# Optimization experiments

Measured on AMD Instinct MI355X. Metric: run time of the kernel, lower is better.

Reference implementation:

```python
import jax, jax.numpy as jnp
import numpy as np

N = 10000
E = 320000
DIM_IN, DIM_H, DIM_OUT, HEADS = 256, 64, 32, 8
NEG_SLOPE = 0.2


def setup_inputs() -> dict:
    key = jax.random.key(0)
    ks = jax.random.split(key, 10)
    x = jax.random.normal(ks[0], (N, DIM_IN), dtype=jnp.float32)
    edge_index = jax.random.randint(ks[1], (2, E), 0, N, dtype=jnp.int64)
    def glorot(k, shape, fan_in):
        return jax.random.normal(k, shape, dtype=jnp.float32) / np.sqrt(fan_in)
    # layer 1: GATv2Conv(256 -> 64, heads=8)
    W1l = glorot(ks[2], (DIM_IN, HEADS * DIM_H), DIM_IN)
    W1r = glorot(ks[3], (DIM_IN, HEADS * DIM_H), DIM_IN)
    att1 = glorot(ks[4], (HEADS, DIM_H), DIM_H)
    b1 = jnp.zeros((HEADS * DIM_H,), dtype=jnp.float32)
    # layer 2: GATv2Conv(512 -> 32, heads=1)
    W2l = glorot(ks[5], (HEADS * DIM_H, DIM_OUT), HEADS * DIM_H)
    W2r = glorot(ks[6], (HEADS * DIM_H, DIM_OUT), HEADS * DIM_H)
    att2 = glorot(ks[7], (1, DIM_OUT), DIM_OUT)
    b2 = jnp.zeros((DIM_OUT,), dtype=jnp.float32)
    return {"x": x, "edge_index": edge_index, "W1l": W1l, "W1r": W1r,
            "att1": att1, "b1": b1, "W2l": W2l, "W2r": W2r, "att2": att2, "b2": b2}


def gatv2_conv(x, src, dst, Wl, Wr, att, bias, heads, out_ch, concat):
    n = x.shape[0]
    xl = (x @ Wl).reshape(n, heads, out_ch)  # source transform
    xr = (x @ Wr).reshape(n, heads, out_ch)  # target transform
    e = jax.nn.leaky_relu(xl[src] + xr[dst], NEG_SLOPE)       # [E,H,C]
    alpha = jnp.einsum('ehc,hc->eh', e, att)                  # [E,H]
    amax = jax.lax.stop_gradient(
        jax.ops.segment_max(alpha, dst, num_segments=n))      # [N,H]
    ex = jnp.exp(alpha - amax[dst])
    denom = jax.ops.segment_sum(ex, dst, num_segments=n)
    alpha = ex / (denom[dst] + 1e-16)
    msg = xl[src] * alpha[..., None]                          # [E,H,C]
    out = jax.ops.segment_sum(msg, dst, num_segments=n)       # [N,H,C]
    out = out.reshape(n, heads * out_ch) if concat else out.mean(axis=1)
    return out + bias


def reference(x, edge_index, W1l, W1r, att1, b1, W2l, W2r, att2, b2):
    n = x.shape[0]
    loops = jnp.arange(n, dtype=edge_index.dtype)
    src = jnp.concatenate([edge_index[0], loops])  # add_self_loops=True (PyG default)
    dst = jnp.concatenate([edge_index[1], loops])
    h = gatv2_conv(x, src, dst, W1l, W1r, att1, b1, HEADS, DIM_H, True)
    h = jax.nn.elu(h)
    h = gatv2_conv(h, src, dst, W2l, W2r, att2, b2, 1, DIM_OUT, True)
    return jax.nn.log_softmax(h, axis=1)
```

## Files before the change

### kernel.cpp

```cpp
#include <hip/hip_runtime.h>
#include <hip/hip_bf16.h>


constexpr int N_NODES = 10000;
constexpr int N_EDGES = 320000;
constexpr int ET      = N_EDGES + N_NODES;
constexpr float NEG_SLOPE = 0.2f;

constexpr int NB_COUNT  = (ET + 255) / 256;
constexpr int NB_CONVX  = (N_NODES * 64) / 256;
constexpr int NB_CONVW  = (1024 * 64) / 256;
constexpr int NB_CONVW2 = (64 * 128) / 256;

typedef __attribute__((ext_vector_type(8))) short short8;
typedef __attribute__((ext_vector_type(8))) unsigned short ushort8_t;
typedef __attribute__((ext_vector_type(4))) float floatx4;

__device__ __forceinline__ float lrelu(float a) {
    return fmaxf(a, NEG_SLOPE * a);
}
__device__ __forceinline__ unsigned short f2bf(float f) {
    unsigned u = __float_as_uint(f);
    unsigned r = u + 0x7FFFu + ((u >> 16) & 1u);
    return (unsigned short)(r >> 16);
}
__device__ __forceinline__ float bf2f(unsigned short h) {
    return __uint_as_float((unsigned)h << 16);
}
__device__ __forceinline__ float red8_dpp(float p) {
    int x;
    x = __builtin_amdgcn_update_dpp(0, __float_as_int(p), 0xB1, 0xF, 0xF, true);
    p += __int_as_float(x);
    x = __builtin_amdgcn_update_dpp(0, __float_as_int(p), 0x4E, 0xF, 0xF, true);
    p += __int_as_float(x);
    x = __builtin_amdgcn_update_dpp(0, __float_as_int(p), 0x141, 0xF, 0xF, true);
    p += __int_as_float(x);
    return p;
}
__device__ __forceinline__ float red8max_dpp(float p) {
    int x;
    x = __builtin_amdgcn_update_dpp(0, __float_as_int(p), 0xB1, 0xF, 0xF, true);
    p = fmaxf(p, __int_as_float(x));
    x = __builtin_amdgcn_update_dpp(0, __float_as_int(p), 0x4E, 0xF, 0xF, true);
    p = fmaxf(p, __int_as_float(x));
    x = __builtin_amdgcn_update_dpp(0, __float_as_int(p), 0x141, 0xF, 0xF, true);
    p = fmaxf(p, __int_as_float(x));
    return p;
}
__device__ __forceinline__ float ror8_add(float p) {
    int x = __builtin_amdgcn_update_dpp(0, __float_as_int(p), 0x128, 0xF, 0xF, true);
    return p + __int_as_float(x);
}


__global__ __launch_bounds__(256) void k_prep(const int* __restrict__ ei,
        int* __restrict__ deg, const float* __restrict__ x,
        unsigned short* __restrict__ A, const float* __restrict__ Wl,
        const float* __restrict__ Wr, unsigned short* __restrict__ Bt,
        const float* __restrict__ W2l, const float* __restrict__ W2r,
        unsigned short* __restrict__ Bt2) {
    int b = blockIdx.x, t = threadIdx.x;
    if (b < NB_COUNT) {
        int e = b * 256 + t;
        if (e >= ET) return;
        int d = (e < N_EDGES) ? ei[N_EDGES + e] : (e - N_EDGES);
        atomicAdd(&deg[d], 1);
    } else if (b < NB_COUNT + NB_CONVX) {
        int idx = (b - NB_COUNT) * 256 + t;
        int m = idx >> 6, kg = (idx & 63) << 2;
        float4 v = *reinterpret_cast<const float4*>(x + (size_t)m * 256 + kg);
        ushort4 hi = make_ushort4(f2bf(v.x), f2bf(v.y), f2bf(v.z), f2bf(v.w));
        ushort4 lo = make_ushort4(f2bf(v.x - bf2f(hi.x)), f2bf(v.y - bf2f(hi.y)),
                                  f2bf(v.z - bf2f(hi.z)), f2bf(v.w - bf2f(hi.w)));
        size_t base = (size_t)m * 512 + kg;
        *reinterpret_cast<ushort4*>(A + base)       = hi;
        *reinterpret_cast<ushort4*>(A + base + 256) = lo;
    } else if (b < NB_COUNT + NB_CONVX + NB_CONVW) {
        int idx = (b - NB_COUNT - NB_CONVX) * 256 + t;
        int n = idx >> 6, kg = (idx & 63) << 2;
        const float* src = (n < 512) ? (Wl + n) : (Wr + (n - 512));
        float v0 = src[(size_t)(kg + 0) * 512];
        float v1 = src[(size_t)(kg + 1) * 512];
        float v2 = src[(size_t)(kg + 2) * 512];
        float v3 = src[(size_t)(kg + 3) * 512];
        ushort4 hi = make_ushort4(f2bf(v0), f2bf(v1), f2bf(v2), f2bf(v3));
        size_t base = (size_t)n * 512 + kg;
        *reinterpret_cast<ushort4*>(Bt + base)       = hi;
        *reinterpret_cast<ushort4*>(Bt + base + 256) = hi;
    } else {
        int idx = (b - NB_COUNT - NB_CONVX - NB_CONVW) * 256 + t;
        int j = idx >> 7, kg = (idx & 127) << 2;
        const float* src = (j < 32) ? (W2l + j) : (W2r + (j - 32));
        float v0 = src[(size_t)(kg + 0) * 32];
        float v1 = src[(size_t)(kg + 1) * 32];
        float v2 = src[(size_t)(kg + 2) * 32];
        float v3 = src[(size_t)(kg + 3) * 32];
        ushort4 hi = make_ushort4(f2bf(v0), f2bf(v1), f2bf(v2), f2bf(v3));
        *reinterpret_cast<ushort4*>(Bt2 + (size_t)j * 512 + kg) = hi;
    }
}


__global__ __launch_bounds__(1024) void k_scan(const int* __restrict__ deg,
                                               int* __restrict__ offs) {
    __shared__ int part[1024];
    const int CH = 10;
    int t = threadIdx.x;
    int base = t * CH;
    int loc[CH];
    int s = 0;
    for (int i = 0; i < CH; ++i) {
        int idx = base + i;
        int v = (idx < N_NODES) ? deg[idx] : 0;
        loc[i] = s; s += v;
    }
    part[t] = s;
    __syncthreads();
    for (int o = 1; o < 1024; o <<= 1) {
        int add = (t >= o) ? part[t - o] : 0;
        __syncthreads();
        part[t] += add;
        __syncthreads();
    }
    int excl = part[t] - s;
    for (int i = 0; i < CH; ++i) {
        int idx = base + i;
        if (idx < N_NODES) offs[idx] = excl + loc[i];
    }
    if (t == 1023) offs[N_NODES] = part[1023];
}

__global__ void k_scatter(const int* __restrict__ ei, const int* __restrict__ offs,
                          int* __restrict__ deg, int* __restrict__ ssrc) {
    int e = blockIdx.x * 256 + threadIdx.x;
    if (e >= ET) return;
    int s, d;
    if (e < N_EDGES) { s = ei[e]; d = ei[N_EDGES + e]; }
    else             { s = d = e - N_EDGES; }
    int pos = offs[d] + atomicAdd(&deg[d], -1) - 1;
    ssrc[pos] = s;
}


__global__ __launch_bounds__(256) void k_mfma1(const unsigned short* __restrict__ A,
        const unsigned short* __restrict__ Bt, unsigned short* __restrict__ xl1b,
        unsigned short* __restrict__ xr1b) {
    __shared__ unsigned short As[128 * 40];
    __shared__ unsigned short Bs[128 * 40];
    int t = threadIdx.x;
    int wave = t >> 6, L = t & 63;
    int wm = wave & 1, wn = wave >> 1;
    int row0 = blockIdx.x * 128, n0 = blockIdx.y * 128;
    int q = L >> 4, rr = L & 15;
    floatx4 acc[4][4];
#pragma unroll
    for (int i = 0; i < 4; ++i)
#pragma unroll
        for (int j = 0; j < 4; ++j) acc[i][j] = (floatx4){0.f, 0.f, 0.f, 0.f};
    int ra = t >> 2,        ka = (t & 3) * 8;
    int rb = (t + 256) >> 2, kb = ((t + 256) & 3) * 8;
    int gma = row0 + ra; gma = (gma < N_NODES) ? gma : (N_NODES - 1);
    int gmb = row0 + rb; gmb = (gmb < N_NODES) ? gmb : (N_NODES - 1);
    for (int kc = 0; kc < 512; kc += 32) {
        __syncthreads();
        *reinterpret_cast<uint4*>(&As[ra * 40 + ka]) =
            *reinterpret_cast<const uint4*>(A + (size_t)gma * 512 + kc + ka);
        *reinterpret_cast<uint4*>(&As[rb * 40 + kb]) =
            *reinterpret_cast<const uint4*>(A + (size_t)gmb * 512 + kc + kb);
        *reinterpret_cast<uint4*>(&Bs[ra * 40 + ka]) =
            *reinterpret_cast<const uint4*>(Bt + (size_t)(n0 + ra) * 512 + kc + ka);
        *reinterpret_cast<uint4*>(&Bs[rb * 40 + kb]) =
            *reinterpret_cast<const uint4*>(Bt + (size_t)(n0 + rb) * 512 + kc + kb);
        __syncthreads();
        short8 af[4], bf[4];
#pragma unroll
        for (int st = 0; st < 4; ++st)
            af[st] = *reinterpret_cast<const short8*>(
                &As[(wm * 64 + st * 16 + rr) * 40 + q * 8]);
#pragma unroll
        for (int st = 0; st < 4; ++st)
            bf[st] = *reinterpret_cast<const short8*>(
                &Bs[(wn * 64 + st * 16 + rr) * 40 + q * 8]);
#pragma unroll
        for (int i = 0; i < 4; ++i)
#pragma unroll
            for (int j = 0; j < 4; ++j)
                acc[i][j] = __builtin_amdgcn_mfma_f32_16x16x32_bf16(
                    af[i], bf[j], acc[i][j], 0, 0, 0);
    }
#pragma unroll
    for (int j = 0; j < 4; ++j) {
        int gc = n0 + wn * 64 + j * 16 + rr;
        unsigned short* dst = (gc < 512) ? xl1b : xr1b;
        int col = (gc < 512) ? gc : (gc - 512);
#pragma unroll
        for (int i = 0; i < 4; ++i)
#pragma unroll
            for (int r = 0; r < 4; ++r) {
                int gr = row0 + wm * 64 + i * 16 + q * 4 + r;
                if (gr < N_NODES)
                    dst[(size_t)gr * 512 + col] = f2bf(acc[i][j][r]);
            }
    }
}

__global__ __launch_bounds__(512) void k_node1f(const int* __restrict__ offs,
        const int* __restrict__ ssrc, const unsigned short* __restrict__ xl1b,
        const unsigned short* __restrict__ xr1b, const float* __restrict__ att1,
        const float* __restrict__ b1, unsigned short* __restrict__ h1b) {
    int n = blockIdx.x;
    int t = threadIdx.x;
    int h = t >> 6, lane = t & 63;
    int beg = offs[n], dcnt = offs[n + 1] - beg;
    int ej = lane >> 3;
    int cg = lane & 7;
    float xrv[8], atv[8];
    {
        ushort8_t xru = *reinterpret_cast<const ushort8_t*>(
            xr1b + (size_t)n * 512 + h * 64 + cg * 8);
        const float* atrow = att1 + h * 64 + cg * 8;
        float4 c0 = *reinterpret_cast<const float4*>(atrow);
        float4 c1 = *reinterpret_cast<const float4*>(atrow + 4);
#pragma unroll
        for (int i = 0; i < 8; ++i) xrv[i] = bf2f(xru[i]);
        atv[0]=c0.x; atv[1]=c0.y; atv[2]=c0.z; atv[3]=c0.w;
        atv[4]=c1.x; atv[5]=c1.y; atv[6]=c1.z; atv[7]=c1.w;
    }
    float l = 0.f;
    float acc8[8];
#pragma unroll
    for (int i = 0; i < 8; ++i) acc8[i] = 0.f;
    const int* sp = ssrc + beg;
    const char* xlbase = reinterpret_cast<const char*>(xl1b) + h * 128 + cg * 16;

    auto ld_off = [&](int i1) -> int {
        int i1c = (i1 < dcnt) ? i1 : (dcnt - 1);
        return sp[i1c] << 10;
    };
    auto ld_row = [&](int off) -> ushort8_t {
        return *reinterpret_cast<const ushort8_t*>(xlbase + off);
    };
    int full = dcnt & ~15;
    ushort8_t uA = ld_row(ld_off(ej));
    ushort8_t uB = ld_row(ld_off(8 + ej));
    int oA1 = ld_off(16 + ej), oB1 = ld_off(24 + ej);
    for (int base = 0; base < full; base += 16) {
        ushort8_t uA1 = ld_row(oA1), uB1 = ld_row(oB1);
        int oA2 = ld_off(base + 32 + ej);
        int oB2 = ld_off(base + 40 + ej);
        float xsA[8], xsB[8];
#pragma unroll
        for (int i = 0; i < 8; ++i) { xsA[i] = bf2f(uA[i]); xsB[i] = bf2f(uB[i]); }
        float pA0 = 0.f, pA1 = 0.f, pB0 = 0.f, pB1 = 0.f;
#pragma unroll
        for (int i = 0; i < 4; ++i) {
            pA0 += lrelu(xsA[i] + xrv[i]) * atv[i];
            pA1 += lrelu(xsA[i + 4] + xrv[i + 4]) * atv[i + 4];
            pB0 += lrelu(xsB[i] + xrv[i]) * atv[i];
            pB1 += lrelu(xsB[i + 4] + xrv[i + 4]) * atv[i + 4];
        }
        float wA = __expf(fminf(red8_dpp(pA0 + pA1), 60.f));
        float wB = __expf(fminf(red8_dpp(pB0 + pB1), 60.f));
        l += wA + wB;
#pragma unroll
        for (int i = 0; i < 8; ++i) acc8[i] += wA * xsA[i] + wB * xsB[i];
        uA = uA1; uB = uB1; oA1 = oA2; oB1 = oB2;
    }
    if (full < dcnt) {
        float xsA[8], xsB[8];
#pragma unroll
        for (int i = 0; i < 8; ++i) { xsA[i] = bf2f(uA[i]); xsB[i] = bf2f(uB[i]); }
        float pA0 = 0.f, pA1 = 0.f, pB0 = 0.f, pB1 = 0.f;
#pragma unroll
        for (int i = 0; i < 4; ++i) {
            pA0 += lrelu(xsA[i] + xrv[i]) * atv[i];
            pA1 += lrelu(xsA[i + 4] + xrv[i + 4]) * atv[i + 4];
            pB0 += lrelu(xsB[i] + xrv[i]) * atv[i];
            pB1 += lrelu(xsB[i + 4] + xrv[i + 4]) * atv[i + 4];
        }
        float pA = red8_dpp(pA0 + pA1);
        float pB = red8_dpp(pB0 + pB1);
        if (full + ej >= dcnt)     pA = -1e30f;
        if (full + 8 + ej >= dcnt) pB = -1e30f;
        float wA = __expf(fminf(pA, 60.f));
        float wB = __expf(fminf(pB, 60.f));
        l += wA + wB;
#pragma unroll
        for (int i = 0; i < 8; ++i) acc8[i] += wA * xsA[i] + wB * xsB[i];
    }
    l = ror8_add(l); l += __shfl_xor(l, 16); l += __shfl_xor(l, 32);
#pragma unroll
    for (int i = 0; i < 8; ++i) {
        acc8[i] = ror8_add(acc8[i]);
        acc8[i] += __shfl_xor(acc8[i], 16);
        acc8[i] += __shfl_xor(acc8[i], 32);
    }
    float inv = 1.f / (l + 1e-16f);
    if (ej == 0) {
        const float* brow = b1 + h * 64 + cg * 8;
        ushort8_t vout;
#pragma unroll
        for (int i = 0; i < 8; ++i) {
            float v = acc8[i] * inv + brow[i];
            v = (v > 0.f) ? v : (__expf(v) - 1.f);
            vout[i] = f2bf(v);
        }
        *reinterpret_cast<ushort8_t*>(
            h1b + (size_t)n * 512 + h * 64 + cg * 8) = vout;
    }
}


__global__ __launch_bounds__(256) void k_mfma2(const unsigned short* __restrict__ h1b,
        const unsigned short* __restrict__ Bt2, float* __restrict__ xw2) {
    __shared__ unsigned short Hs[128 * 40];
    __shared__ unsigned short Ws[64 * 40];
    int t = threadIdx.x;
    int wave = t >> 6, L = t & 63;
    int row0 = blockIdx.x * 128;
    int q = L >> 4, rr = L & 15;
    floatx4 acc[2][4];
#pragma unroll
    for (int i = 0; i < 2; ++i)
#pragma unroll
        for (int j = 0; j < 4; ++j) acc[i][j] = (floatx4){0.f, 0.f, 0.f, 0.f};
    int ra = t >> 2,        ka = (t & 3) * 8;
    int rb = (t + 256) >> 2, kb = ((t + 256) & 3) * 8;
    int gma = row0 + ra; gma = (gma < N_NODES) ? gma : (N_NODES - 1);
    int gmb = row0 + rb; gmb = (gmb < N_NODES) ? gmb : (N_NODES - 1);
    for (int kc = 0; kc < 512; kc += 32) {
        __syncthreads();
        *reinterpret_cast<uint4*>(&Hs[ra * 40 + ka]) =
            *reinterpret_cast<const uint4*>(h1b + (size_t)gma * 512 + kc + ka);
        *reinterpret_cast<uint4*>(&Hs[rb * 40 + kb]) =
            *reinterpret_cast<const uint4*>(h1b + (size_t)gmb * 512 + kc + kb);
        *reinterpret_cast<uint4*>(&Ws[ra * 40 + ka]) =
            *reinterpret_cast<const uint4*>(Bt2 + (size_t)(ra & 63) * 512 + kc + ka);
        __syncthreads();
        short8 af[2], bf[4];
#pragma unroll
        for (int i = 0; i < 2; ++i)
            af[i] = *reinterpret_cast<const short8*>(
                &Hs[(wave * 32 + i * 16 + rr) * 40 + q * 8]);
#pragma unroll
        for (int j = 0; j < 4; ++j)
            bf[j] = *reinterpret_cast<const short8*>(
                &Ws[(j * 16 + rr) * 40 + q * 8]);
#pragma unroll
        for (int i = 0; i < 2; ++i)
#pragma unroll
            for (int j = 0; j < 4; ++j)
                acc[i][j] = __builtin_amdgcn_mfma_f32_16x16x32_bf16(
                    af[i], bf[j], acc[i][j], 0, 0, 0);
    }
#pragma unroll
    for (int j = 0; j < 4; ++j) {
        int gc = j * 16 + rr;
#pragma unroll
        for (int i = 0; i < 2; ++i)
#pragma unroll
            for (int r = 0; r < 4; ++r) {
                int gr = row0 + wave * 32 + i * 16 + q * 4 + r;
                if (gr < N_NODES) xw2[(size_t)gr * 64 + gc] = acc[i][j][r];
            }
    }
}

__global__ __launch_bounds__(256) void k_node2f(const int* __restrict__ offs,
        const int* __restrict__ ssrc, const float* __restrict__ xw2,
        const float* __restrict__ att2, const float* __restrict__ b2,
        float* __restrict__ out) {
    int t = threadIdx.x;
    int wave = t >> 6, lane = t & 63;
    int n = blockIdx.x * 4 + wave;
    if (n >= N_NODES) return;
    int ej = lane >> 3;
    int cg = lane & 7;
    int beg = offs[n], dcnt = offs[n + 1] - beg;
    float4 xr = *reinterpret_cast<const float4*>(
                    xw2 + (size_t)n * 64 + 32 + cg * 4);
    float4 at = *reinterpret_cast<const float4*>(att2 + cg * 4);
    float l = 0.f;
    float4 ac = {0.f, 0.f, 0.f, 0.f};
    const int* sp = ssrc + beg;
    const char* xwbase = reinterpret_cast<const char*>(xw2) + cg * 16;
    auto ld_off = [&](int i1) -> int {
        int i1c = (i1 < dcnt) ? i1 : (dcnt - 1);
        return sp[i1c] << 8;
    };
    auto ld_row = [&](int off) -> float4 {
        return *reinterpret_cast<const float4*>(xwbase + off);
    };
    int full = dcnt & ~15;
    float4 uA = ld_row(ld_off(ej));
    float4 uB = ld_row(ld_off(8 + ej));
    int oA1 = ld_off(16 + ej), oB1 = ld_off(24 + ej);
    for (int base = 0; base < full; base += 16) {
        float4 uA1 = ld_row(oA1), uB1 = ld_row(oB1);
        int oA2 = ld_off(base + 32 + ej);
        int oB2 = ld_off(base + 40 + ej);
        float pA0 = lrelu(uA.x + xr.x) * at.x + lrelu(uA.z + xr.z) * at.z;
        float pA1 = lrelu(uA.y + xr.y) * at.y + lrelu(uA.w + xr.w) * at.w;
        float pB0 = lrelu(uB.x + xr.x) * at.x + lrelu(uB.z + xr.z) * at.z;
        float pB1 = lrelu(uB.y + xr.y) * at.y + lrelu(uB.w + xr.w) * at.w;
        float wA = __expf(fminf(red8_dpp(pA0 + pA1), 60.f));
        float wB = __expf(fminf(red8_dpp(pB0 + pB1), 60.f));
        l += wA + wB;
        ac.x += wA * uA.x + wB * uB.x;
        ac.y += wA * uA.y + wB * uB.y;
        ac.z += wA * uA.z + wB * uB.z;
        ac.w += wA * uA.w + wB * uB.w;
        uA = uA1; uB = uB1; oA1 = oA2; oB1 = oB2;
    }
    if (full < dcnt) {
        float pA0 = lrelu(uA.x + xr.x) * at.x + lrelu(uA.z + xr.z) * at.z;
        float pA1 = lrelu(uA.y + xr.y) * at.y + lrelu(uA.w + xr.w) * at.w;
        float pB0 = lrelu(uB.x + xr.x) * at.x + lrelu(uB.z + xr.z) * at.z;
        float pB1 = lrelu(uB.y + xr.y) * at.y + lrelu(uB.w + xr.w) * at.w;
        float pA = red8_dpp(pA0 + pA1);
        float pB = red8_dpp(pB0 + pB1);
        if (full + ej >= dcnt)     pA = -1e30f;
        if (full + 8 + ej >= dcnt) pB = -1e30f;
        float wA = __expf(fminf(pA, 60.f));
        float wB = __expf(fminf(pB, 60.f));
        l += wA + wB;
        ac.x += wA * uA.x + wB * uB.x;
        ac.y += wA * uA.y + wB * uB.y;
        ac.z += wA * uA.z + wB * uB.z;
        ac.w += wA * uA.w + wB * uB.w;
    }
    l = ror8_add(l); l += __shfl_xor(l, 16); l += __shfl_xor(l, 32);
    ac.x = ror8_add(ac.x); ac.x += __shfl_xor(ac.x, 16); ac.x += __shfl_xor(ac.x, 32);
    ac.y = ror8_add(ac.y); ac.y += __shfl_xor(ac.y, 16); ac.y += __shfl_xor(ac.y, 32);
    ac.z = ror8_add(ac.z); ac.z += __shfl_xor(ac.z, 16); ac.z += __shfl_xor(ac.z, 32);
    ac.w = ror8_add(ac.w); ac.w += __shfl_xor(ac.w, 16); ac.w += __shfl_xor(ac.w, 32);
    float inv = 1.f / (l + 1e-16f);
    float4 bb = *reinterpret_cast<const float4*>(b2 + cg * 4);
    float4 v;
    v.x = ac.x * inv + bb.x; v.y = ac.y * inv + bb.y;
    v.z = ac.z * inv + bb.z; v.w = ac.w * inv + bb.w;
    float mx = red8max_dpp(fmaxf(fmaxf(v.x, v.y), fmaxf(v.z, v.w)));
    float se = red8_dpp(__expf(v.x - mx) + __expf(v.y - mx)
                      + __expf(v.z - mx) + __expf(v.w - mx));
    float ls = __logf(se);
    v.x = v.x - mx - ls; v.y = v.y - mx - ls;
    v.z = v.z - mx - ls; v.w = v.w - mx - ls;
    if (ej == 0)
        *reinterpret_cast<float4*>(out + (size_t)n * 32 + cg * 4) = v;
}


extern "C" void kernel_launch(void* const* d_in, const int* in_sizes, int n_in,
                              void* d_out, int out_size, void* d_ws, size_t ws_size,
                              hipStream_t stream) {
    (void)in_sizes; (void)n_in; (void)out_size; (void)ws_size;
    const float* x    = (const float*)d_in[0];
    const int*   ei   = (const int*)d_in[1];
    const float* W1l  = (const float*)d_in[2];
    const float* W1r  = (const float*)d_in[3];
    const float* att1 = (const float*)d_in[4];
    const float* b1   = (const float*)d_in[5];
    const float* W2l  = (const float*)d_in[6];
    const float* W2r  = (const float*)d_in[7];
    const float* att2 = (const float*)d_in[8];
    const float* b2   = (const float*)d_in[9];
    float* outp = (float*)d_out;

    char* ws = (char*)d_ws;
    size_t o = 0;
    auto alloc = [&](size_t bytes) {
        char* p = ws + o;
        o = (o + bytes + 255) & ~(size_t)255;
        return p;
    };
    unsigned short* xl1b = (unsigned short*)alloc((size_t)N_NODES * 512 * 2);
    unsigned short* xr1b = (unsigned short*)alloc((size_t)N_NODES * 512 * 2);
    unsigned short* h1b  = (unsigned short*)alloc((size_t)N_NODES * 512 * 2);
    float* xw2    = (float*)alloc((size_t)N_NODES * 64 * 4);
    unsigned short* Abf = (unsigned short*)alloc((size_t)N_NODES * 512 * 2);
    unsigned short* Bbf = (unsigned short*)alloc((size_t)1024 * 512 * 2);
    unsigned short* Bt2 = (unsigned short*)alloc((size_t)64 * 512 * 2);
    int*   deg    = (int*)alloc((size_t)N_NODES * 4);
    int*   offs   = (int*)alloc((size_t)(N_NODES + 1) * 4);
    int*   ssrc   = (int*)alloc((size_t)ET * 4);

    hipMemsetAsync(deg, 0, (size_t)N_NODES * 4, stream);

    k_prep   <<<NB_COUNT + NB_CONVX + NB_CONVW + NB_CONVW2, 256, 0, stream>>>(
                 ei, deg, x, Abf, W1l, W1r, Bbf, W2l, W2r, Bt2);
    k_scan   <<<1,                    1024, 0, stream>>>(deg, offs);
    k_scatter<<<(ET + 255) / 256,      256, 0, stream>>>(ei, offs, deg, ssrc);
    k_mfma1  <<<dim3(79, 8),           256, 0, stream>>>(Abf, Bbf, xl1b, xr1b);
    k_node1f <<<N_NODES,               512, 0, stream>>>(offs, ssrc, xl1b, xr1b, att1, b1, h1b);
    k_mfma2  <<<79,                    256, 0, stream>>>(h1b, Bt2, xw2);
    k_node2f <<<(N_NODES + 3) / 4,     256, 0, stream>>>(offs, ssrc, xw2, att2, b2, outp);
}
```

Baseline: 237.9 us.

## Map one wave per node in layer-1 aggregation and halve layer-2 GEMM tile

The layer-1 attention/aggregation kernel used to spend a 512-thread block (one wave per head) on each node, with 8 edges processed in parallel per wave. It now gives each node a single wave whose 64 lanes cover all 512 channels and walk the edges one at a time, reading whole 1 KB source rows. This removes the cross-edge shuffle reductions, the tail masking and the idle lanes on low-degree nodes. In exchange there is less memory-level parallelism per wave, since only two rows are prefetched, and high-degree nodes form a longer serial chain. Separately, the layer-2 MFMA GEMM tile is cut from 128 to 64 rows, doubling the block count so more CUs are busy.

Measured after the change: 230.0 us. 1.03x faster.

```diff
diff --git a/kernel.cpp b/kernel.cpp
--- a/kernel.cpp
+++ b/kernel.cpp
@@ -204,21 +204,20 @@
     }
 }
 
-__global__ __launch_bounds__(512) void k_node1f(const int* __restrict__ offs,
+__global__ __launch_bounds__(256) void k_node1f(const int* __restrict__ offs,
         const int* __restrict__ ssrc, const unsigned short* __restrict__ xl1b,
         const unsigned short* __restrict__ xr1b, const float* __restrict__ att1,
         const float* __restrict__ b1, unsigned short* __restrict__ h1b) {
-    int n = blockIdx.x;
     int t = threadIdx.x;
-    int h = t >> 6, lane = t & 63;
+    int wave = t >> 6, lane = t & 63;
+    int n = blockIdx.x * 4 + wave;
+    if (n >= N_NODES) return;
     int beg = offs[n], dcnt = offs[n + 1] - beg;
-    int ej = lane >> 3;
-    int cg = lane & 7;
     float xrv[8], atv[8];
     {
         ushort8_t xru = *reinterpret_cast<const ushort8_t*>(
-            xr1b + (size_t)n * 512 + h * 64 + cg * 8);
-        const float* atrow = att1 + h * 64 + cg * 8;
+            xr1b + (size_t)n * 512 + lane * 8);
+        const float* atrow = att1 + lane * 8;
         float4 c0 = *reinterpret_cast<const float4*>(atrow);
         float4 c1 = *reinterpret_cast<const float4*>(atrow + 4);
 #pragma unroll
@@ -231,138 +230,84 @@
 #pragma unroll
     for (int i = 0; i < 8; ++i) acc8[i] = 0.f;
     const int* sp = ssrc + beg;
-    const char* xlbase = reinterpret_cast<const char*>(xl1b) + h * 128 + cg * 16;
-
-    auto ld_off = [&](int i1) -> int {
-        int i1c = (i1 < dcnt) ? i1 : (dcnt - 1);
-        return sp[i1c] << 10;
+    const char* xlbase = reinterpret_cast<const char*>(xl1b) + lane * 16;
+    auto ld_off = [&](int i) -> int {
+        int ic = (i < dcnt) ? i : (dcnt - 1);
+        return sp[ic] << 10;
     };
     auto ld_row = [&](int off) -> ushort8_t {
         return *reinterpret_cast<const ushort8_t*>(xlbase + off);
     };
-    int full = dcnt & ~15;
-    ushort8_t uA = ld_row(ld_off(ej));
-    ushort8_t uB = ld_row(ld_off(8 + ej));
-    int oA1 = ld_off(16 + ej), oB1 = ld_off(24 + ej);
-    for (int base = 0; base < full; base += 16) {
-        ushort8_t uA1 = ld_row(oA1), uB1 = ld_row(oB1);
-        int oA2 = ld_off(base + 32 + ej);
-        int oB2 = ld_off(base + 40 + ej);
-        float xsA[8], xsB[8];
-#pragma unroll
-        for (int i = 0; i < 8; ++i) { xsA[i] = bf2f(uA[i]); xsB[i] = bf2f(uB[i]); }
-        float pA0 = 0.f, pA1 = 0.f, pB0 = 0.f, pB1 = 0.f;
-#pragma unroll
-        for (int i = 0; i < 4; ++i) {
-            pA0 += lrelu(xsA[i] + xrv[i]) * atv[i];
-            pA1 += lrelu(xsA[i + 4] + xrv[i + 4]) * atv[i + 4];
-            pB0 += lrelu(xsB[i] + xrv[i]) * atv[i];
-            pB1 += lrelu(xsB[i + 4] + xrv[i + 4]) * atv[i + 4];
+    ushort8_t u0 = ld_row(ld_off(0));
+    ushort8_t u1 = ld_row(ld_off(1));
+    for (int i = 0; i < dcnt; ++i) {
+        ushort8_t u2 = ld_row(ld_off(i + 2));
+        float xs[8];
+#pragma unroll
+        for (int j = 0; j < 8; ++j) xs[j] = bf2f(u0[j]);
+        float p0 = 0.f, p1 = 0.f;
+#pragma unroll
+        for (int j = 0; j < 4; ++j) {
+            p0 += lrelu(xs[j] + xrv[j]) * atv[j];
+            p1 += lrelu(xs[j + 4] + xrv[j + 4]) * atv[j + 4];
         }
-        float wA = __expf(fminf(red8_dpp(pA0 + pA1), 60.f));
-        float wB = __expf(fminf(red8_dpp(pB0 + pB1), 60.f));
-        l += wA + wB;
-#pragma unroll
-        for (int i = 0; i < 8; ++i) acc8[i] += wA * xsA[i] + wB * xsB[i];
-        uA = uA1; uB = uB1; oA1 = oA2; oB1 = oB2;
-    }
-    if (full < dcnt) {
-        float xsA[8], xsB[8];
-#pragma unroll
-        for (int i = 0; i < 8; ++i) { xsA[i] = bf2f(uA[i]); xsB[i] = bf2f(uB[i]); }
-        float pA0 = 0.f, pA1 = 0.f, pB0 = 0.f, pB1 = 0.f;
-#pragma unroll
-        for (int i = 0; i < 4; ++i) {
-            pA0 += lrelu(xsA[i] + xrv[i]) * atv[i];
-            pA1 += lrelu(xsA[i + 4] + xrv[i + 4]) * atv[i + 4];
-            pB0 += lrelu(xsB[i] + xrv[i]) * atv[i];
-            pB1 += lrelu(xsB[i + 4] + xrv[i + 4]) * atv[i + 4];
-        }
-        float pA = red8_dpp(pA0 + pA1);
-        float pB = red8_dpp(pB0 + pB1);
-        if (full + ej >= dcnt)     pA = -1e30f;
-        if (full + 8 + ej >= dcnt) pB = -1e30f;
-        float wA = __expf(fminf(pA, 60.f));
-        float wB = __expf(fminf(pB, 60.f));
-        l += wA + wB;
-#pragma unroll
-        for (int i = 0; i < 8; ++i) acc8[i] += wA * xsA[i] + wB * xsB[i];
-    }
-    l = ror8_add(l); l += __shfl_xor(l, 16); l += __shfl_xor(l, 32);
-#pragma unroll
-    for (int i = 0; i < 8; ++i) {
-        acc8[i] = ror8_add(acc8[i]);
-        acc8[i] += __shfl_xor(acc8[i], 16);
-        acc8[i] += __shfl_xor(acc8[i], 32);
+        float p = red8_dpp(p0 + p1);
+        float w = __expf(fminf(p, 60.f));
+        l += w;
+#pragma unroll
+        for (int j = 0; j < 8; ++j) acc8[j] += w * xs[j];
+        u0 = u1; u1 = u2;
     }
     float inv = 1.f / (l + 1e-16f);
-    if (ej == 0) {
-        const float* brow = b1 + h * 64 + cg * 8;
-        ushort8_t vout;
-#pragma unroll
-        for (int i = 0; i < 8; ++i) {
-            float v = acc8[i] * inv + brow[i];
-            v = (v > 0.f) ? v : (__expf(v) - 1.f);
-            vout[i] = f2bf(v);
-        }
-        *reinterpret_cast<ushort8_t*>(
-            h1b + (size_t)n * 512 + h * 64 + cg * 8) = vout;
-    }
+    const float* brow = b1 + lane * 8;
+    ushort8_t vout;
+#pragma unroll
+    for (int j = 0; j < 8; ++j) {
+        float v = acc8[j] * inv + brow[j];
+        v = (v > 0.f) ? v : (__expf(v) - 1.f);
+        vout[j] = f2bf(v);
+    }
+    *reinterpret_cast<ushort8_t*>(h1b + (size_t)n * 512 + lane * 8) = vout;
 }
 
 
 __global__ __launch_bounds__(256) void k_mfma2(const unsigned short* __restrict__ h1b,
         const unsigned short* __restrict__ Bt2, float* __restrict__ xw2) {
-    __shared__ unsigned short Hs[128 * 40];
+    __shared__ unsigned short Hs[64 * 40];
     __shared__ unsigned short Ws[64 * 40];
     int t = threadIdx.x;
     int wave = t >> 6, L = t & 63;
-    int row0 = blockIdx.x * 128;
+    int row0 = blockIdx.x * 64;
     int q = L >> 4, rr = L & 15;
-    floatx4 acc[2][4];
-#pragma unroll
-    for (int i = 0; i < 2; ++i)
-#pragma unroll
-        for (int j = 0; j < 4; ++j) acc[i][j] = (floatx4){0.f, 0.f, 0.f, 0.f};
-    int ra = t >> 2,        ka = (t & 3) * 8;
-    int rb = (t + 256) >> 2, kb = ((t + 256) & 3) * 8;
+    floatx4 acc[4];
+#pragma unroll
+    for (int j = 0; j < 4; ++j) acc[j] = (floatx4){0.f, 0.f, 0.f, 0.f};
+    int ra = t >> 2, ka = (t & 3) * 8;
     int gma = row0 + ra; gma = (gma < N_NODES) ? gma : (N_NODES - 1);
-    int gmb = row0 + rb; gmb = (gmb < N_NODES) ? gmb : (N_NODES - 1);
     for (int kc = 0; kc < 512; kc += 32) {
         __syncthreads();
         *reinterpret_cast<uint4*>(&Hs[ra * 40 + ka]) =
             *reinterpret_cast<const uint4*>(h1b + (size_t)gma * 512 + kc + ka);
-        *reinterpret_cast<uint4*>(&Hs[rb * 40 + kb]) =
-            *reinterpret_cast<const uint4*>(h1b + (size_t)gmb * 512 + kc + kb);
         *reinterpret_cast<uint4*>(&Ws[ra * 40 + ka]) =
-            *reinterpret_cast<const uint4*>(Bt2 + (size_t)(ra & 63) * 512 + kc + ka);
-        __syncthreads();
-        short8 af[2], bf[4];
-#pragma unroll
-        for (int i = 0; i < 2; ++i)
-            af[i] = *reinterpret_cast<const short8*>(
-                &Hs[(wave * 32 + i * 16 + rr) * 40 + q * 8]);
-#pragma unroll
-        for (int j = 0; j < 4; ++j)
-            bf[j] = *reinterpret_cast<const short8*>(
+            *reinterpret_cast<const uint4*>(Bt2 + (size_t)ra * 512 + kc + ka);
+        __syncthreads();
+        short8 af = *reinterpret_cast<const short8*>(
+            &Hs[(wave * 16 + rr) * 40 + q * 8]);
+#pragma unroll
+        for (int j = 0; j < 4; ++j) {
+            short8 bf = *reinterpret_cast<const short8*>(
                 &Ws[(j * 16 + rr) * 40 + q * 8]);
-#pragma unroll
-        for (int i = 0; i < 2; ++i)
-#pragma unroll
-            for (int j = 0; j < 4; ++j)
-                acc[i][j] = __builtin_amdgcn_mfma_f32_16x16x32_bf16(
-                    af[i], bf[j], acc[i][j], 0, 0, 0);
+            acc[j] = __builtin_amdgcn_mfma_f32_16x16x32_bf16(af, bf, acc[j], 0, 0, 0);
+        }
     }
 #pragma unroll
     for (int j = 0; j < 4; ++j) {
         int gc = j * 16 + rr;
 #pragma unroll
-        for (int i = 0; i < 2; ++i)
-#pragma unroll
-            for (int r = 0; r < 4; ++r) {
-                int gr = row0 + wave * 32 + i * 16 + q * 4 + r;
-                if (gr < N_NODES) xw2[(size_t)gr * 64 + gc] = acc[i][j][r];
-            }
+        for (int r = 0; r < 4; ++r) {
+            int gr = row0 + wave * 16 + q * 4 + r;
+            if (gr < N_NODES) xw2[(size_t)gr * 64 + gc] = acc[j][r];
+        }
     }
 }
 
@@ -491,7 +436,7 @@
     k_scan   <<<1,                    1024, 0, stream>>>(deg, offs);
     k_scatter<<<(ET + 255) / 256,      256, 0, stream>>>(ei, offs, deg, ssrc);
     k_mfma1  <<<dim3(79, 8),           256, 0, stream>>>(Abf, Bbf, xl1b, xr1b);
-    k_node1f <<<N_NODES,               512, 0, stream>>>(offs, ssrc, xl1b, xr1b, att1, b1, h1b);
-    k_mfma2  <<<79,                    256, 0, stream>>>(h1b, Bt2, xw2);
+    k_node1f <<<(N_NODES + 3) / 4,     256, 0, stream>>>(offs, ssrc, xl1b, xr1b, att1, b1, h1b);
+    k_mfma2  <<<(N_NODES + 63) / 64,   256, 0, stream>>>(h1b, Bt2, xw2);
     k_node2f <<<(N_NODES + 3) / 4,     256, 0, stream>>>(offs, ssrc, xw2, att2, b2, outp);
 }
```
